# Optimization experiments

Hardware: AMD Instinct MI355X
Metric: run time of the kernel (lower is better)

Reference implementation:

```python
import jax, jax.numpy as jnp
import numpy as np

BN_EPS = 1e-5


def conv1x1(x, w):
    # x: [B,C,H,W], w: [O,C] (1x1 conv kernel squeezed)
    return jnp.einsum('bchw,oc->bohw', x, w)


def setup_inputs() -> dict:
    key = jax.random.key(0)
    ks = jax.random.split(key, 16)
    B, Cin, H, W = 8, 768, 64, 64
    MID, INTER, OUT = 256, 128, 20
    s = lambda fan_in: 1.0 / np.sqrt(fan_in)
    inp = {
        'x1': jax.random.normal(ks[0], (B, Cin, H, W), jnp.float32),
        'x2': jax.random.normal(ks[1], (B, Cin, H, W), jnp.float32),
        'w_conv': jax.random.normal(ks[2], (MID, Cin), jnp.float32) * s(Cin),
        'w_theta': jax.random.normal(ks[3], (INTER, MID), jnp.float32) * s(MID),
        'w_phi': jax.random.normal(ks[4], (INTER, MID), jnp.float32) * s(MID),
        'w_g': jax.random.normal(ks[5], (INTER, MID), jnp.float32) * s(MID),
        'w_W': jax.random.normal(ks[6], (MID, INTER), jnp.float32) * s(INTER),
        'b_W': jax.random.normal(ks[7], (MID,), jnp.float32) * 0.01,
        'bn_gamma': jax.random.uniform(ks[8], (MID,), jnp.float32, 0.5, 1.5),
        'bn_beta': jax.random.normal(ks[9], (MID,), jnp.float32) * 0.01,
        'bn_mean': jax.random.normal(ks[10], (MID,), jnp.float32) * 0.01,
        'bn_var': jax.random.uniform(ks[11], (MID,), jnp.float32, 0.5, 1.5),
        'w_out': jax.random.normal(ks[12], (OUT, MID), jnp.float32) * s(MID),
        'b_out': jax.random.normal(ks[13], (OUT,), jnp.float32) * 0.01,
    }
    return inp


def reference(x1, x2, w_conv, w_theta, w_phi, w_g, w_W, b_W,
              bn_gamma, bn_beta, bn_mean, bn_var, w_out, b_out):
    # shared 1x1 projection (applied to x1 because x1.size(1)==x2.size(1))
    x1p = conv1x1(x1, w_conv)            # [B,MID,H,W]
    x2p = conv1x1(x2, w_conv)            # [B,MID,H,W]
    B, MID, H, W = x1p.shape
    N = H * W
    inter = w_theta.shape[0]

    # embedded-Gaussian non-local: theta from x1, phi/g from x2
    theta = conv1x1(x1p, w_theta).reshape(B, inter, N)   # [B,I,N]
    phi = conv1x1(x2p, w_phi).reshape(B, inter, N)       # [B,I,N]
    g = conv1x1(x2p, w_g).reshape(B, inter, N)           # [B,I,N]

    f = jnp.einsum('bci,bcj->bij', theta, phi)           # [B,N,N]
    attn = jax.nn.softmax(f, axis=-1)
    y = jnp.einsum('bij,bcj->bci', attn, g)              # [B,I,N]
    y = y.reshape(B, inter, H, W)

    # W: 1x1 conv + BatchNorm (eval mode, running stats), residual with x1p
    Wy = conv1x1(y, w_W) + b_W[None, :, None, None]
    inv = bn_gamma * jax.lax.rsqrt(bn_var + BN_EPS)
    Wy = Wy * inv[None, :, None, None] + (bn_beta - bn_mean * inv)[None, :, None, None]
    z = Wy + x1p

    out = conv1x1(z, w_out) + b_out[None, :, None, None]  # [B,20,H,W]
    return out
```

## Files before the change

kernel.cpp:

```cpp
#include <hip/hip_runtime.h>

typedef _Float16 half8 __attribute__((ext_vector_type(8)));
typedef _Float16 half4v __attribute__((ext_vector_type(4)));
typedef float floatx4 __attribute__((ext_vector_type(4)));

#define MFMA16(a,b,c) __builtin_amdgcn_mfma_f32_16x16x32_f16((a),(b),(c),0,0,0)


__global__ __launch_bounds__(256) void k_convert(
    const float* __restrict__ w_conv, const float* __restrict__ w_theta,
    const float* __restrict__ w_phi, const float* __restrict__ w_g,
    _Float16* __restrict__ w_conv_h, _Float16* __restrict__ w_theta_h,
    _Float16* __restrict__ w_phi_h, _Float16* __restrict__ w_g_h)
{
    int tid = blockIdx.x * 256 + threadIdx.x;
    int nth = gridDim.x * 256;
    for (int i = tid; i < 256 * 768; i += nth) w_conv_h[i] = (_Float16)w_conv[i];
    for (int i = tid; i < 128 * 256; i += nth) {
        w_theta_h[i] = (_Float16)w_theta[i];
        w_phi_h[i]   = (_Float16)w_phi[i];
        w_g_h[i]     = (_Float16)w_g[i];
    }
}

__global__ __launch_bounds__(256) void k_fold(
    const float* __restrict__ w_W, const float* __restrict__ b_W,
    const float* __restrict__ gamma, const float* __restrict__ beta,
    const float* __restrict__ mean, const float* __restrict__ var,
    const float* __restrict__ w_out, const float* __restrict__ b_out,
    _Float16* __restrict__ Acat, float* __restrict__ c0)
{
    int u = blockIdx.x, t = threadIdx.x;
    __shared__ float woi[256];
    __shared__ float wcv[256];
    if (u >= 20) {
        for (int k = t; k < 384; k += 256) Acat[u * 384 + k] = (_Float16)0.f;
        if (t == 0) c0[u] = 0.f;
        return;
    }
    {
        float inv = gamma[t] * rsqrtf(var[t] + 1e-5f);
        float wo = w_out[u * 256 + t];
        woi[t] = wo * inv;
        wcv[t] = wo * (b_W[t] * inv + beta[t] - mean[t] * inv);
    }
    __syncthreads();
    for (int k = t; k < 384; k += 256) {
        float v;
        if (k < 128) {
            v = 0.f;
            for (int o = 0; o < 256; ++o) v += woi[o] * w_W[o * 128 + k];
        } else {
            v = w_out[u * 256 + (k - 128)];
        }
        Acat[u * 384 + k] = (_Float16)v;
    }
    if (t == 0) {
        float s = b_out[u];
        for (int o = 0; o < 256; ++o) s += wcv[o];
        c0[u] = s;
    }
}

__global__ __launch_bounds__(256) void k_transpose(
    const float* __restrict__ x1, const float* __restrict__ x2,
    _Float16* __restrict__ x1t, _Float16* __restrict__ x2t)
{
    int z = blockIdx.z >> 3, b = blockIdx.z & 7;
    const float* X = (z ? x2 : x1) + (size_t)b * 768 * 4096;
    _Float16* XT = (z ? x2t : x1t) + (size_t)b * 4096 * 768;
    int n0 = blockIdx.x * 64, c0 = blockIdx.y * 64;
    __shared__ float tile[64][65];
    int t = threadIdx.x;
    {
        int c = t >> 2, ns = (t & 3) * 16;
        const float* src = X + (size_t)(c0 + c) * 4096 + n0 + ns;
#pragma unroll
        for (int e = 0; e < 4; ++e)
            *(float4*)&tile[c][ns + e * 4] = *(const float4*)(src + e * 4);
    }
    __syncthreads();
    {
        int n = t >> 2, cs = (t & 3) * 16;
        _Float16 outv[16];
#pragma unroll
        for (int e = 0; e < 16; ++e) outv[e] = (_Float16)tile[cs + e][n];
        _Float16* dst = XT + (size_t)(n0 + n) * 768 + c0 + cs;
        *(half8*)(dst)     = *(half8*)&outv[0];
        *(half8*)(dst + 8) = *(half8*)&outv[8];
    }
}

__global__ __launch_bounds__(256) void k_gemm_nt(
    const _Float16* __restrict__ A, const _Float16* __restrict__ B,
    _Float16* __restrict__ C, int K, int ldc, int perm)
{
    int m0 = blockIdx.x * 128, n0 = blockIdx.y * 128;
    __shared__ _Float16 As[128][72];
    __shared__ _Float16 Bs[128][72];
    int t = threadIdx.x, wave = t >> 6, lane = t & 63;
    int wm = (wave >> 1) * 64, wn = (wave & 1) * 64;
    int fl = lane & 15, fq = lane >> 4;
    int sr = t >> 2, sc = (t & 3) * 8;

    floatx4 acc[4][4];
#pragma unroll
    for (int i = 0; i < 4; ++i)
#pragma unroll
        for (int j = 0; j < 4; ++j) acc[i][j] = (floatx4){0.f, 0.f, 0.f, 0.f};

    for (int ko = 0; ko < K; ko += 32) {
        __syncthreads();
        half8 av0 = *(const half8*)(A + (size_t)(m0 + sr) * K + ko + sc);
        half8 av1 = *(const half8*)(A + (size_t)(m0 + sr + 64) * K + ko + sc);
        half8 bv0 = *(const half8*)(B + (size_t)(n0 + sr) * K + ko + sc);
        half8 bv1 = *(const half8*)(B + (size_t)(n0 + sr + 64) * K + ko + sc);
        *(half8*)&As[sr][sc] = av0;
        *(half8*)&As[sr + 64][sc] = av1;
        *(half8*)&Bs[sr][sc] = bv0;
        *(half8*)&Bs[sr + 64][sc] = bv1;
        __syncthreads();
        half8 af[4], bf[4];
#pragma unroll
        for (int i = 0; i < 4; ++i) af[i] = *(const half8*)&As[wm + 16 * i + fl][8 * fq];
#pragma unroll
        for (int j = 0; j < 4; ++j) bf[j] = *(const half8*)&Bs[wn + 16 * j + fl][8 * fq];
#pragma unroll
        for (int i = 0; i < 4; ++i)
#pragma unroll
            for (int j = 0; j < 4; ++j) acc[i][j] = MFMA16(af[i], bf[j], acc[i][j]);
    }
#pragma unroll
    for (int i = 0; i < 4; ++i)
#pragma unroll
        for (int j = 0; j < 4; ++j) {
            int row = m0 + wm + 16 * i + 4 * fq;
            int col = n0 + wn + 16 * j + fl;
            int cs2 = perm ? ((col & ~31) | (((col >> 2) & 3) << 3) |
                              (((col >> 4) & 1) << 2) | (col & 3))
                           : col;
#pragma unroll
            for (int r = 0; r < 4; ++r)
                C[(size_t)(row + r) * ldc + cs2] = (_Float16)acc[i][j][r];
        }
}

__global__ __launch_bounds__(256, 2) void k_attn2(
    const _Float16* __restrict__ theta_t, const _Float16* __restrict__ phi_t,
    const _Float16* __restrict__ gbuf, float* __restrict__ Opart,
    float* __restrict__ Mp, float* __restrict__ Lp)
{
    int bi = blockIdx.x;
    int b = bi & 7;
    int r5 = bi >> 3;
    int iblk = r5 & 31, jh = r5 >> 5;
    int i0g = b * 4096 + iblk * 128;
    int t = threadIdx.x, wave = t >> 6, lane = t & 63;
    int fl = lane & 15, fq = lane >> 4;
    int iw = i0g + wave * 32;

    __shared__ _Float16 Ks[64][132];
    __shared__ _Float16 Gs[128][68];

    half8 qf[2][4];
#pragma unroll
    for (int it = 0; it < 2; ++it)
#pragma unroll
        for (int kc = 0; kc < 4; ++kc)
            qf[it][kc] = *(const half8*)(theta_t +
                (size_t)(iw + 16 * it + fl) * 128 + kc * 32 + 8 * fq);

    floatx4 O[8][2];
#pragma unroll
    for (int ct = 0; ct < 8; ++ct)
#pragma unroll
        for (int it = 0; it < 2; ++it) O[ct][it] = (floatx4){0.f, 0.f, 0.f, 0.f};
    float m[2] = {-1e30f, -1e30f}, l[2] = {0.f, 0.f};

    int jbase = b * 4096 + jh * 2048;
    for (int jc = 0; jc < 32; ++jc) {
        int j0g = jbase + jc * 64;
        __syncthreads();
        {
            int jr = t >> 2, cs = (t & 3) * 32;
            const _Float16* src = phi_t + (size_t)(j0g + jr) * 128 + cs;
#pragma unroll
            for (int e = 0; e < 4; ++e)
                *(half8*)&Ks[jr][cs + 8 * e] = *(const half8*)(src + 8 * e);
        }
        {
            int c = t >> 1, js = (t & 1) * 32;
            const _Float16* src = gbuf + (size_t)c * 32768 + j0g + js;
#pragma unroll
            for (int e = 0; e < 4; ++e)
                *(half8*)&Gs[c][js + 8 * e] = *(const half8*)(src + 8 * e);
        }
        __syncthreads();

        floatx4 S[4][2];
#pragma unroll
        for (int jt = 0; jt < 4; ++jt)
#pragma unroll
            for (int it = 0; it < 2; ++it) S[jt][it] = (floatx4){0.f, 0.f, 0.f, 0.f};
#pragma unroll
        for (int kc = 0; kc < 4; ++kc)
#pragma unroll
            for (int jt = 0; jt < 4; ++jt) {
                half8 af = *(const half8*)&Ks[16 * jt + fl][kc * 32 + 8 * fq];
                S[jt][0] = MFMA16(af, qf[0][kc], S[jt][0]);
                S[jt][1] = MFMA16(af, qf[1][kc], S[jt][1]);
            }

        half8 pk[2][2];
        float alpha[2];
#pragma unroll
        for (int it = 0; it < 2; ++it) {
            float mx = S[0][it][0];
#pragma unroll
            for (int jt = 0; jt < 4; ++jt)
#pragma unroll
                for (int rr = 0; rr < 4; ++rr) mx = fmaxf(mx, S[jt][it][rr]);
            mx = fmaxf(mx, __shfl_xor(mx, 16, 64));
            mx = fmaxf(mx, __shfl_xor(mx, 32, 64));
            float mn = fmaxf(m[it], mx);
            alpha[it] = __expf(m[it] - mn);
            m[it] = mn;
            float sum = 0.f;
#pragma unroll
            for (int jt = 0; jt < 4; ++jt)
#pragma unroll
                for (int rr = 0; rr < 4; ++rr) {
                    float pv = __expf(S[jt][it][rr] - mn);
                    S[jt][it][rr] = pv;
                    sum += pv;
                }
            sum += __shfl_xor(sum, 16, 64);
            sum += __shfl_xor(sum, 32, 64);
            l[it] = l[it] * alpha[it] + sum;
#pragma unroll
            for (int kj = 0; kj < 2; ++kj)
#pragma unroll
                for (int e = 0; e < 8; ++e)
                    pk[it][kj][e] = (_Float16)S[2 * kj + (e >> 2)][it][e & 3];
        }
#pragma unroll
        for (int ct = 0; ct < 8; ++ct)
#pragma unroll
            for (int it = 0; it < 2; ++it)
#pragma unroll
                for (int rr = 0; rr < 4; ++rr) O[ct][it][rr] *= alpha[it];
#pragma unroll
        for (int kj = 0; kj < 2; ++kj)
#pragma unroll
            for (int ct = 0; ct < 8; ++ct) {
                half8 gf = *(const half8*)&Gs[16 * ct + fl][kj * 32 + 8 * fq];
                O[ct][0] = MFMA16(gf, pk[0][kj], O[ct][0]);
                O[ct][1] = MFMA16(gf, pk[1][kj], O[ct][1]);
            }
    }

#pragma unroll
    for (int it = 0; it < 2; ++it) {
        size_t ig = (size_t)jh * 32768 + iw + 16 * it + fl;
#pragma unroll
        for (int ct = 0; ct < 8; ++ct)
            *(floatx4*)&Opart[ig * 128 + 16 * ct + 4 * fq] = O[ct][it];
        if (fq == 0) { Mp[ig] = m[it]; Lp[ig] = l[it]; }
    }
}

__global__ __launch_bounds__(256) void k_merge(
    const float* __restrict__ Opart, const float* __restrict__ Mp,
    const float* __restrict__ Lp, _Float16* __restrict__ y_t)
{
    int g = blockIdx.x * 256 + threadIdx.x;
    int i = g >> 5, cb = (g & 31) * 4;
    float m0 = Mp[i], m1 = Mp[32768 + i];
    float l0 = Lp[i], l1 = Lp[32768 + i];
    float M = fmaxf(m0, m1);
    float w0 = __expf(m0 - M), w1 = __expf(m1 - M);
    float inv = 1.f / (w0 * l0 + w1 * l1);
    w0 *= inv; w1 *= inv;
    float4 o0 = *(const float4*)&Opart[(size_t)i * 128 + cb];
    float4 o1 = *(const float4*)&Opart[(size_t)(32768 + i) * 128 + cb];
    half4v y;
    y[0] = (_Float16)(w0 * o0.x + w1 * o1.x);
    y[1] = (_Float16)(w0 * o0.y + w1 * o1.y);
    y[2] = (_Float16)(w0 * o0.z + w1 * o1.z);
    y[3] = (_Float16)(w0 * o0.w + w1 * o1.w);
    *(half4v*)&y_t[(size_t)i * 128 + cb] = y;
}

__global__ __launch_bounds__(256) void k_out(
    const _Float16* __restrict__ y_t, const _Float16* __restrict__ x1p_t,
    const _Float16* __restrict__ Acat, const float* __restrict__ c0,
    float* __restrict__ out)
{
    int n0 = blockIdx.x * 128;
    __shared__ _Float16 As[32][72];
    __shared__ _Float16 Bs[128][72];
    __shared__ float c0s[32];
    int t = threadIdx.x, wave = t >> 6, lane = t & 63;
    int fl = lane & 15, fq = lane >> 4;
    int wn = wave * 32;
    if (t < 32) c0s[t] = c0[t];

    floatx4 acc[2][2];
#pragma unroll
    for (int i = 0; i < 2; ++i)
#pragma unroll
        for (int j = 0; j < 2; ++j) acc[i][j] = (floatx4){0.f, 0.f, 0.f, 0.f};

    for (int ko = 0; ko < 12; ++ko) {
        int kg = ko * 32;
        __syncthreads();
        {
            int n = t >> 1, ks = (t & 1) * 16;
            const _Float16* src = (kg < 128)
                ? y_t + (size_t)(n0 + n) * 128 + kg + ks
                : x1p_t + (size_t)(n0 + n) * 256 + (kg - 128) + ks;
            *(half8*)&Bs[n][ks]     = *(const half8*)src;
            *(half8*)&Bs[n][ks + 8] = *(const half8*)(src + 8);
        }
        if (t < 128) {
            int mm = t >> 2, ks = (t & 3) * 8;
            *(half8*)&As[mm][ks] = *(const half8*)(Acat + mm * 384 + kg + ks);
        }
        __syncthreads();
        half8 af[2], bf[2];
#pragma unroll
        for (int mt = 0; mt < 2; ++mt) af[mt] = *(const half8*)&As[16 * mt + fl][8 * fq];
#pragma unroll
        for (int nt = 0; nt < 2; ++nt) bf[nt] = *(const half8*)&Bs[wn + 16 * nt + fl][8 * fq];
#pragma unroll
        for (int mt = 0; mt < 2; ++mt)
#pragma unroll
            for (int nt = 0; nt < 2; ++nt) acc[mt][nt] = MFMA16(af[mt], bf[nt], acc[mt][nt]);
    }
#pragma unroll
    for (int mt = 0; mt < 2; ++mt)
#pragma unroll
        for (int nt = 0; nt < 2; ++nt)
#pragma unroll
            for (int r = 0; r < 4; ++r) {
                int u = 16 * mt + 4 * fq + r;
                if (u < 20) {
                    int ng = n0 + wn + 16 * nt + fl;
                    int b = ng >> 12, n = ng & 4095;
                    out[((size_t)b * 20 + u) * 4096 + n] = acc[mt][nt][r] + c0s[u];
                }
            }
}

extern "C" void kernel_launch(void* const* d_in, const int* in_sizes, int n_in,
                              void* d_out, int out_size, void* d_ws, size_t ws_size,
                              hipStream_t stream)
{
    const float* x1     = (const float*)d_in[0];
    const float* x2     = (const float*)d_in[1];
    const float* w_conv = (const float*)d_in[2];
    const float* w_theta= (const float*)d_in[3];
    const float* w_phi  = (const float*)d_in[4];
    const float* w_g    = (const float*)d_in[5];
    const float* w_W    = (const float*)d_in[6];
    const float* b_W    = (const float*)d_in[7];
    const float* gamma  = (const float*)d_in[8];
    const float* beta   = (const float*)d_in[9];
    const float* mean   = (const float*)d_in[10];
    const float* var    = (const float*)d_in[11];
    const float* w_out  = (const float*)d_in[12];
    const float* b_out  = (const float*)d_in[13];
    float* out = (float*)d_out;
    char* ws = (char*)d_ws;

    _Float16* x1t      = (_Float16*)(ws + 0);
    _Float16* x2t      = (_Float16*)(ws + 50331648);
    _Float16* x1p      = (_Float16*)(ws + 100663296);
    _Float16* x2p      = (_Float16*)(ws + 117440512);
    _Float16* theta_t  = (_Float16*)(ws + 0);
    _Float16* phi_t    = (_Float16*)(ws + 8388608);
    _Float16* gbuf     = (_Float16*)(ws + 16777216);
    _Float16* y_t      = (_Float16*)(ws + 25165824);
    float*    Opart    = (float*)   (ws + 33554432);
    float*    Mp       = (float*)   (ws + 67108864);
    float*    Lp       = (float*)   (ws + 67371008);
    _Float16* w_conv_h = (_Float16*)(ws + 134217728);
    _Float16* w_theta_h= (_Float16*)(ws + 134610944);
    _Float16* w_phi_h  = (_Float16*)(ws + 134676480);
    _Float16* w_g_h    = (_Float16*)(ws + 134742016);
    _Float16* Acat     = (_Float16*)(ws + 134807552);
    float*    c0       = (float*)   (ws + 134832128);

    k_convert<<<64, 256, 0, stream>>>(w_conv, w_theta, w_phi, w_g,
                                      w_conv_h, w_theta_h, w_phi_h, w_g_h);
    k_fold<<<32, 256, 0, stream>>>(w_W, b_W, gamma, beta, mean, var,
                                   w_out, b_out, Acat, c0);
    k_transpose<<<dim3(64, 12, 16), 256, 0, stream>>>(x1, x2, x1t, x2t);
    k_gemm_nt<<<dim3(256, 2), 256, 0, stream>>>(x1t, w_conv_h, x1p, 768, 256, 0);
    k_gemm_nt<<<dim3(256, 2), 256, 0, stream>>>(x2t, w_conv_h, x2p, 768, 256, 0);
    k_gemm_nt<<<dim3(256, 1), 256, 0, stream>>>(x1p, w_theta_h, theta_t, 256, 128, 0);
    k_gemm_nt<<<dim3(256, 1), 256, 0, stream>>>(x2p, w_phi_h, phi_t, 256, 128, 0);
    k_gemm_nt<<<dim3(1, 256), 256, 0, stream>>>(w_g_h, x2p, gbuf, 256, 32768, 1);
    k_attn2<<<512, 256, 0, stream>>>(theta_t, phi_t, gbuf, Opart, Mp, Lp);
    k_merge<<<4096, 256, 0, stream>>>(Opart, Mp, Lp, y_t);
    k_out<<<256, 256, 0, stream>>>(y_t, x1p, Acat, c0, out);
    (void)in_sizes; (void)n_in; (void)out_size; (void)ws_size;
}
```

Baseline: 457.3 us.

## Split attention KV four ways, use exp2 with prescaled theta, LDS-direct GEMM loads

The attention kernel now splits the key dimension into four partitions instead of two, doubling the grid and raising the occupancy hint. The merge kernel is generalised to four partials. Theta weights are prescaled by log2(e) so softmax can use the native exp2, and the output rescale is skipped when no row max changes in the wave. The projection GEMMs switch to a new kernel that loads tiles with global_load_lds straight into unpadded shared memory, which risks LDS bank conflicts, and the merge cost and partial-buffer traffic grow with four splits.

Result: slower. 553.7 us (+21.1%).

```diff
diff --git a/kernel.cpp b/kernel.cpp
--- a/kernel.cpp
+++ b/kernel.cpp
@@ -5,7 +5,14 @@
 typedef float floatx4 __attribute__((ext_vector_type(4)));
 
 #define MFMA16(a,b,c) __builtin_amdgcn_mfma_f32_16x16x32_f16((a),(b),(c),0,0,0)
-
+#define EXP2F(x) __builtin_amdgcn_exp2f(x)
+
+
+__device__ inline void gl_lds16(const _Float16* g, _Float16* l) {
+    __builtin_amdgcn_global_load_lds(
+        (const __attribute__((address_space(1))) unsigned int*)g,
+        (__attribute__((address_space(3))) unsigned int*)l, 16, 0, 0);
+}
 
 __global__ __launch_bounds__(256) void k_convert(
     const float* __restrict__ w_conv, const float* __restrict__ w_theta,
@@ -17,7 +24,7 @@
     int nth = gridDim.x * 256;
     for (int i = tid; i < 256 * 768; i += nth) w_conv_h[i] = (_Float16)w_conv[i];
     for (int i = tid; i < 128 * 256; i += nth) {
-        w_theta_h[i] = (_Float16)w_theta[i];
+        w_theta_h[i] = (_Float16)(w_theta[i] * 1.44269504f);
         w_phi_h[i]   = (_Float16)w_phi[i];
         w_g_h[i]     = (_Float16)w_g[i];
     }
@@ -91,6 +98,63 @@
     }
 }
 
+__global__ __launch_bounds__(256) void k_gemm_lds(
+    const _Float16* __restrict__ A, const _Float16* __restrict__ B,
+    _Float16* __restrict__ C, int K, int ldc)
+{
+    int m0 = blockIdx.x * 128, n0 = blockIdx.y * 128;
+    __shared__ _Float16 As[128 * 64];
+    __shared__ _Float16 Bs[128 * 64];
+    int t = threadIdx.x, wave = t >> 6, lane = t & 63;
+    int wm = (wave >> 1) * 64, wn = (wave & 1) * 64;
+    int fl = lane & 15, fq = lane >> 4;
+    int lrow = wave * 8 + (lane >> 3);
+    int lkoff = (lane & 7) * 8;
+
+    floatx4 acc[4][4];
+#pragma unroll
+    for (int i = 0; i < 4; ++i)
+#pragma unroll
+        for (int j = 0; j < 4; ++j) acc[i][j] = (floatx4){0.f, 0.f, 0.f, 0.f};
+
+    for (int ko = 0; ko < K; ko += 64) {
+        __syncthreads();
+#pragma unroll
+        for (int q = 0; q < 4; ++q) {
+            int row = q * 32 + lrow;
+            gl_lds16(A + (size_t)(m0 + row) * K + ko + lkoff,
+                     As + q * 2048 + wave * 512);
+            gl_lds16(B + (size_t)(n0 + row) * K + ko + lkoff,
+                     Bs + q * 2048 + wave * 512);
+        }
+        __syncthreads();
+#pragma unroll
+        for (int kc = 0; kc < 2; ++kc) {
+            half8 af[4], bf[4];
+#pragma unroll
+            for (int i = 0; i < 4; ++i)
+                af[i] = *(const half8*)&As[(wm + 16 * i + fl) * 64 + kc * 32 + 8 * fq];
+#pragma unroll
+            for (int j = 0; j < 4; ++j)
+                bf[j] = *(const half8*)&Bs[(wn + 16 * j + fl) * 64 + kc * 32 + 8 * fq];
+#pragma unroll
+            for (int i = 0; i < 4; ++i)
+#pragma unroll
+                for (int j = 0; j < 4; ++j) acc[i][j] = MFMA16(af[i], bf[j], acc[i][j]);
+        }
+    }
+#pragma unroll
+    for (int i = 0; i < 4; ++i)
+#pragma unroll
+        for (int j = 0; j < 4; ++j) {
+            int row = m0 + wm + 16 * i + 4 * fq;
+            int col = n0 + wn + 16 * j + fl;
+#pragma unroll
+            for (int r = 0; r < 4; ++r)
+                C[(size_t)(row + r) * ldc + col] = (_Float16)acc[i][j][r];
+        }
+}
+
 __global__ __launch_bounds__(256) void k_gemm_nt(
     const _Float16* __restrict__ A, const _Float16* __restrict__ B,
     _Float16* __restrict__ C, int K, int ldc, int perm)
@@ -145,15 +209,15 @@
         }
 }
 
-__global__ __launch_bounds__(256, 2) void k_attn2(
+__global__ __launch_bounds__(256, 4) void k_attn3(
     const _Float16* __restrict__ theta_t, const _Float16* __restrict__ phi_t,
     const _Float16* __restrict__ gbuf, float* __restrict__ Opart,
     float* __restrict__ Mp, float* __restrict__ Lp)
 {
     int bi = blockIdx.x;
     int b = bi & 7;
-    int r5 = bi >> 3;
-    int iblk = r5 & 31, jh = r5 >> 5;
+    int r = bi >> 3;
+    int iblk = r & 31, jh = r >> 5;
     int i0g = b * 4096 + iblk * 128;
     int t = threadIdx.x, wave = t >> 6, lane = t & 63;
     int fl = lane & 15, fq = lane >> 4;
@@ -177,8 +241,8 @@
         for (int it = 0; it < 2; ++it) O[ct][it] = (floatx4){0.f, 0.f, 0.f, 0.f};
     float m[2] = {-1e30f, -1e30f}, l[2] = {0.f, 0.f};
 
-    int jbase = b * 4096 + jh * 2048;
-    for (int jc = 0; jc < 32; ++jc) {
+    int jbase = b * 4096 + jh * 1024;
+    for (int jc = 0; jc < 16; ++jc) {
         int j0g = jbase + jc * 64;
         __syncthreads();
         {
@@ -211,44 +275,54 @@
                 S[jt][1] = MFMA16(af, qf[1][kc], S[jt][1]);
             }
 
+        float mx[2];
+#pragma unroll
+        for (int it = 0; it < 2; ++it) {
+            float v = S[0][it][0];
+#pragma unroll
+            for (int jt = 0; jt < 4; ++jt)
+#pragma unroll
+                for (int rr = 0; rr < 4; ++rr) v = fmaxf(v, S[jt][it][rr]);
+            v = fmaxf(v, __shfl_xor(v, 16, 64));
+            v = fmaxf(v, __shfl_xor(v, 32, 64));
+            mx[it] = v;
+        }
+        float mn0 = fmaxf(m[0], mx[0]), mn1 = fmaxf(m[1], mx[1]);
+        bool up = (mn0 > m[0]) || (mn1 > m[1]);
+        float a0 = EXP2F(m[0] - mn0), a1 = EXP2F(m[1] - mn1);
+        m[0] = mn0; m[1] = mn1;
+
         half8 pk[2][2];
-        float alpha[2];
 #pragma unroll
         for (int it = 0; it < 2; ++it) {
-            float mx = S[0][it][0];
+            float mn = it ? mn1 : mn0;
+            float sum = 0.f;
 #pragma unroll
             for (int jt = 0; jt < 4; ++jt)
 #pragma unroll
-                for (int rr = 0; rr < 4; ++rr) mx = fmaxf(mx, S[jt][it][rr]);
-            mx = fmaxf(mx, __shfl_xor(mx, 16, 64));
-            mx = fmaxf(mx, __shfl_xor(mx, 32, 64));
-            float mn = fmaxf(m[it], mx);
-            alpha[it] = __expf(m[it] - mn);
-            m[it] = mn;
-            float sum = 0.f;
-#pragma unroll
-            for (int jt = 0; jt < 4; ++jt)
-#pragma unroll
                 for (int rr = 0; rr < 4; ++rr) {
-                    float pv = __expf(S[jt][it][rr] - mn);
+                    float pv = EXP2F(S[jt][it][rr] - mn);
                     S[jt][it][rr] = pv;
                     sum += pv;
                 }
             sum += __shfl_xor(sum, 16, 64);
             sum += __shfl_xor(sum, 32, 64);
-            l[it] = l[it] * alpha[it] + sum;
+            l[it] = l[it] * (it ? a1 : a0) + sum;
 #pragma unroll
             for (int kj = 0; kj < 2; ++kj)
 #pragma unroll
                 for (int e = 0; e < 8; ++e)
                     pk[it][kj][e] = (_Float16)S[2 * kj + (e >> 2)][it][e & 3];
         }
-#pragma unroll
-        for (int ct = 0; ct < 8; ++ct)
-#pragma unroll
-            for (int it = 0; it < 2; ++it)
-#pragma unroll
-                for (int rr = 0; rr < 4; ++rr) O[ct][it][rr] *= alpha[it];
+        if (__ballot(up) != 0ull) {
+#pragma unroll
+            for (int ct = 0; ct < 8; ++ct)
+#pragma unroll
+                for (int rr = 0; rr < 4; ++rr) {
+                    O[ct][0][rr] *= a0;
+                    O[ct][1][rr] *= a1;
+                }
+        }
 #pragma unroll
         for (int kj = 0; kj < 2; ++kj)
 #pragma unroll
@@ -275,19 +349,32 @@
 {
     int g = blockIdx.x * 256 + threadIdx.x;
     int i = g >> 5, cb = (g & 31) * 4;
-    float m0 = Mp[i], m1 = Mp[32768 + i];
-    float l0 = Lp[i], l1 = Lp[32768 + i];
-    float M = fmaxf(m0, m1);
-    float w0 = __expf(m0 - M), w1 = __expf(m1 - M);
-    float inv = 1.f / (w0 * l0 + w1 * l1);
-    w0 *= inv; w1 *= inv;
-    float4 o0 = *(const float4*)&Opart[(size_t)i * 128 + cb];
-    float4 o1 = *(const float4*)&Opart[(size_t)(32768 + i) * 128 + cb];
+    float mk[4], lk[4];
+    float M = -1e30f;
+#pragma unroll
+    for (int k = 0; k < 4; ++k) {
+        mk[k] = Mp[k * 32768 + i];
+        lk[k] = Lp[k * 32768 + i];
+        M = fmaxf(M, mk[k]);
+    }
+    float w[4], den = 0.f;
+#pragma unroll
+    for (int k = 0; k < 4; ++k) {
+        w[k] = EXP2F(mk[k] - M);
+        den += w[k] * lk[k];
+    }
+    float inv = 1.f / den;
+    float acc[4] = {0.f, 0.f, 0.f, 0.f};
+#pragma unroll
+    for (int k = 0; k < 4; ++k) {
+        float4 o = *(const float4*)&Opart[((size_t)k * 32768 + i) * 128 + cb];
+        float wk = w[k] * inv;
+        acc[0] += wk * o.x; acc[1] += wk * o.y;
+        acc[2] += wk * o.z; acc[3] += wk * o.w;
+    }
     half4v y;
-    y[0] = (_Float16)(w0 * o0.x + w1 * o1.x);
-    y[1] = (_Float16)(w0 * o0.y + w1 * o1.y);
-    y[2] = (_Float16)(w0 * o0.z + w1 * o1.z);
-    y[3] = (_Float16)(w0 * o0.w + w1 * o1.w);
+#pragma unroll
+    for (int e = 0; e < 4; ++e) y[e] = (_Float16)acc[e];
     *(half4v*)&y_t[(size_t)i * 128 + cb] = y;
 }
 
@@ -382,8 +469,8 @@
     _Float16* gbuf     = (_Float16*)(ws + 16777216);
     _Float16* y_t      = (_Float16*)(ws + 25165824);
     float*    Opart    = (float*)   (ws + 33554432);
-    float*    Mp       = (float*)   (ws + 67108864);
-    float*    Lp       = (float*)   (ws + 67371008);
+    float*    Mp       = (float*)   (ws + 117440512);
+    float*    Lp       = (float*)   (ws + 117964800);
     _Float16* w_conv_h = (_Float16*)(ws + 134217728);
     _Float16* w_theta_h= (_Float16*)(ws + 134610944);
     _Float16* w_phi_h  = (_Float16*)(ws + 134676480);
@@ -396,12 +483,12 @@
     k_fold<<<32, 256, 0, stream>>>(w_W, b_W, gamma, beta, mean, var,
                                    w_out, b_out, Acat, c0);
     k_transpose<<<dim3(64, 12, 16), 256, 0, stream>>>(x1, x2, x1t, x2t);
-    k_gemm_nt<<<dim3(256, 2), 256, 0, stream>>>(x1t, w_conv_h, x1p, 768, 256, 0);
-    k_gemm_nt<<<dim3(256, 2), 256, 0, stream>>>(x2t, w_conv_h, x2p, 768, 256, 0);
-    k_gemm_nt<<<dim3(256, 1), 256, 0, stream>>>(x1p, w_theta_h, theta_t, 256, 128, 0);
-    k_gemm_nt<<<dim3(256, 1), 256, 0, stream>>>(x2p, w_phi_h, phi_t, 256, 128, 0);
+    k_gemm_lds<<<dim3(256, 2), 256, 0, stream>>>(x1t, w_conv_h, x1p, 768, 256);
+    k_gemm_lds<<<dim3(256, 2), 256, 0, stream>>>(x2t, w_conv_h, x2p, 768, 256);
+    k_gemm_lds<<<dim3(256, 1), 256, 0, stream>>>(x1p, w_theta_h, theta_t, 256, 128);
+    k_gemm_lds<<<dim3(256, 1), 256, 0, stream>>>(x2p, w_phi_h, phi_t, 256, 128);
     k_gemm_nt<<<dim3(1, 256), 256, 0, stream>>>(w_g_h, x2p, gbuf, 256, 32768, 1);
-    k_attn2<<<512, 256, 0, stream>>>(theta_t, phi_t, gbuf, Opart, Mp, Lp);
+    k_attn3<<<1024, 256, 0, stream>>>(theta_t, phi_t, gbuf, Opart, Mp, Lp);
     k_merge<<<4096, 256, 0, stream>>>(Opart, Mp, Lp, y_t);
     k_out<<<256, 256, 0, stream>>>(y_t, x1p, Acat, c0, out);
     (void)in_sizes; (void)n_in; (void)out_size; (void)ws_size;
```
